# Optimization experiments

Measured on AMD Instinct MI355X. Metric: run time of the kernel, lower is better.

## Reference

```python
import jax, jax.numpy as jnp
import numpy as np
import math

B, N, IN_DIM, HID, HEADS, K, NCLS = 4, 8192, 1024, 512, 8, 16, 2


def setup_inputs() -> dict:
    key = jax.random.key(0)
    ks = jax.random.split(key, 20)
    s = 0.02
    return {
        "inputs": jax.random.normal(ks[0], (B, N, IN_DIM), jnp.float32),
        "W_feat": jax.random.normal(ks[1], (IN_DIM, HID), jnp.float32) * s,
        "b_feat": jnp.zeros((HID,), jnp.float32),
        "w_enc": jax.random.normal(ks[2], (HID, 1), jnp.float32) * s,
        "b_enc": jnp.zeros((1,), jnp.float32),
        "cls_token": jax.random.normal(ks[3], (1, 1, HID), jnp.float32) * s,
        "conv_w": jax.random.normal(ks[4], (HID, 1, 3, 3), jnp.float32) * s,  # depthwise
        "conv_b": jnp.zeros((HID,), jnp.float32),
        "Wq": jax.random.normal(ks[5], (HID, HID), jnp.float32) * s,
        "bq": jnp.zeros((HID,), jnp.float32),
        "Wk": jax.random.normal(ks[6], (HID, HID), jnp.float32) * s,
        "bk": jnp.zeros((HID,), jnp.float32),
        "Wv": jax.random.normal(ks[7], (HID, HID), jnp.float32) * s,
        "bv": jnp.zeros((HID,), jnp.float32),
        "Wo": jax.random.normal(ks[8], (HID, HID), jnp.float32) * s,
        "bo": jnp.zeros((HID,), jnp.float32),
        "Wc": jax.random.normal(ks[9], (HID, NCLS), jnp.float32) * s,
        "bc": jnp.zeros((NCLS,), jnp.float32),
    }


def reference(inputs, W_feat, b_feat, w_enc, b_enc, cls_token, conv_w, conv_b,
              Wq, bq, Wk, bk, Wv, bv, Wo, bo, Wc, bc):
    # ---- feature projection: [B,N,IN] -> [B,N,HID]
    x = inputs @ W_feat + b_feat

    # ---- recalib(option='max'): sigmoid scores, top-k gather, mean -> Q [B,1,HID]
    scores = jax.nn.sigmoid(jnp.squeeze(x @ w_enc + b_enc, -1))  # [B,N]
    _, idx = jax.lax.top_k(scores, K)                             # [B,K]
    topk = jnp.take_along_axis(x, idx[:, :, None], axis=1)        # [B,K,HID]
    Q = jnp.mean(topk, axis=1, keepdims=True)                     # [B,1,HID]

    # ---- shift + act
    x = jax.nn.relu(x - Q)

    # ---- pad to square grid and run depthwise 3x3 conv with residual
    _H = int(math.ceil(math.sqrt(N)))                             # 91
    add = _H * _H - N
    x = jnp.concatenate([x, x[:, :add]], axis=1)                  # [B, _H*_H, HID]
    feat = jnp.transpose(x, (0, 2, 1)).reshape(B, HID, _H, _H)    # [B,C,H,W]
    conv = jax.lax.conv_general_dilated(
        feat, conv_w, window_strides=(1, 1), padding="SAME",
        feature_group_count=HID)
    feat = conv + conv_b[None, :, None, None] + feat
    x = jnp.transpose(feat.reshape(B, HID, _H * _H), (0, 2, 1))   # [B,_H*_H,HID]

    # ---- prepend cls token
    cls = jnp.broadcast_to(cls_token, (B, 1, HID))
    x = jnp.concatenate([cls, x], axis=1)                         # [B,S,HID]

    # ---- MAB(Q, x): multi-head attention with scale 1/sqrt(dim_V)
    d = HID // HEADS
    q = (Q @ Wq + bq).reshape(B, 1, HEADS, d)
    kk = (x @ Wk + bk).reshape(B, -1, HEADS, d)
    v = (x @ Wv + bv).reshape(B, -1, HEADS, d)
    logits_a = jnp.einsum('bqhd,bkhd->bhqk', q, kk) / math.sqrt(HID)
    A = jax.nn.softmax(logits_a, axis=-1)                         # [B,h,1,S]
    O = q + jnp.einsum('bhqk,bkhd->bqhd', A, v)                   # [B,1,h,d]
    O = O.reshape(B, 1, HID)
    O = O + jax.nn.relu(O @ Wo + bo)
    bag = O[:, 0]                                                 # squeeze(1) -> [B,HID]

    return bag @ Wc + bc                                          # logits [B,NCLS]
```

## Files before the change

### kernel.cpp

```cpp
#include <hip/hip_runtime.h>
#include <math.h>

#define BB 4
#define NN 8192
#define IND 1024
#define HID 512
#define HEADS 8
#define KSEL 16
#define NCLS 2
#define HH 91
#define NPIX 8281
#define NTOK 8282
#define MROWS 32768

typedef short short8 __attribute__((ext_vector_type(8)));
typedef float floatx4 __attribute__((ext_vector_type(4)));

__device__ __forceinline__ unsigned short f2bf(float f) {
  union { float f; unsigned u; } v; v.f = f;
  unsigned r = (v.u + 0x7FFFu + ((v.u >> 16) & 1u)) >> 16;
  return (unsigned short)r;
}
__device__ __forceinline__ float bf2f(unsigned short h) {
  union { unsigned u; float f; } v; v.u = ((unsigned)h) << 16;
  return v.f;
}

__device__ __forceinline__ void gld16(const unsigned short* g, void* l) {
  typedef __attribute__((address_space(1))) const void GV;
  typedef __attribute__((address_space(3))) void LV;
  __builtin_amdgcn_global_load_lds((GV*)g, (LV*)l, 16, 0, 0);
}

__global__ void k_u(const float* __restrict__ W, const float* __restrict__ we,
                    float* __restrict__ u) {
  int wave = threadIdx.x >> 6, lane = threadIdx.x & 63;
  int k = blockIdx.x * 4 + wave;
  const float* wr = W + (long)k * HID + lane * 8;
  const float* wer = we + lane * 8;
  float a = 0.f;
#pragma unroll
  for (int i = 0; i < 8; ++i) a = fmaf(wr[i], wer[i], a);
  for (int off = 32; off; off >>= 1) a += __shfl_down(a, off);
  if (lane == 0) u[k] = a;
}

__global__ void k_wt(const float* __restrict__ W, unsigned short* __restrict__ Wt) {
  __shared__ unsigned short s[64][68];
  int kt = blockIdx.x * 64, nt = blockIdx.y * 64;
  int tid = threadIdx.x;
#pragma unroll
  for (int i = 0; i < 16; ++i) {
    int idx = tid + i * 256;
    int kk2 = idx >> 6, nn2 = idx & 63;
    s[nn2][kk2] = f2bf(W[(long)(kt + kk2) * HID + nt + nn2]);
  }
  __syncthreads();
#pragma unroll
  for (int i = 0; i < 16; ++i) {
    int idx = tid + i * 256;
    int nn2 = idx >> 6, kk2 = idx & 63;
    Wt[(long)(nt + nn2) * IND + kt + kk2] = s[nn2][kk2];
  }
}

__global__ void k_cvt(const float* __restrict__ in, const float* __restrict__ u,
                      unsigned short* __restrict__ abf, float* __restrict__ slog) {
  __shared__ float su[IND];
  int tid = threadIdx.x;
  for (int i = tid; i < IND; i += 256) su[i] = u[i];
  __syncthreads();
  int wave = tid >> 6, lane = tid & 63;
  long row = (long)blockIdx.x * 4 + wave;
  const float* ip = in + row * IND;
  unsigned short* op = abf + row * IND;
  float acc = 0.f;
#pragma unroll
  for (int p = 0; p < 4; ++p) {
    int k = p * 256 + lane * 4;
    float4 v = *(const float4*)(ip + k);
    ushort4 o;
    o.x = f2bf(v.x); o.y = f2bf(v.y); o.z = f2bf(v.z); o.w = f2bf(v.w);
    *(ushort4*)(op + k) = o;
    acc += v.x * su[k] + v.y * su[k + 1] + v.z * su[k + 2] + v.w * su[k + 3];
  }
  for (int off = 32; off; off >>= 1) acc += __shfl_down(acc, off);
  if (lane == 0) slog[row] = acc;
}

__global__ __launch_bounds__(512) void k_gemm(const unsigned short* __restrict__ A,
                                              const unsigned short* __restrict__ Bt,
                                              const float* __restrict__ bias,
                                              unsigned short* __restrict__ X) {
  __shared__ unsigned short sA[128 * 32];
  __shared__ unsigned short sB[256 * 32];
  int tid = threadIdx.x;
  int wave = tid >> 6, lane = tid & 63;
  long m0 = (long)blockIdx.x * 128;
  int n0 = blockIdx.y * 256;
  int wm = (wave >> 2) * 64, wn = (wave & 3) * 64;
  int lm = lane & 15, lk = (lane >> 4) * 8;
  floatx4 acc[4][4];
#pragma unroll
  for (int i = 0; i < 4; ++i)
#pragma unroll
    for (int j = 0; j < 4; ++j) acc[i][j] = (floatx4){0.f, 0.f, 0.f, 0.f};

  const unsigned short* gA = A + (m0 + (tid >> 2)) * IND + (tid & 3) * 8;
  const unsigned short* gB = Bt + (long)(n0 + (tid >> 2)) * IND + (tid & 3) * 8;
  char* sAc = (char*)sA + wave * 1024;
  char* sBc = (char*)sB + wave * 1024;

  for (int k0 = 0; k0 < IND; k0 += 32) {
    gld16(gA + k0, sAc);
    gld16(gB + k0, sBc);
    gld16(gB + k0 + 128 * IND, sBc + 8192);
    __syncthreads();
    short8 af[4], bfr[4];
#pragma unroll
    for (int i = 0; i < 4; ++i)
      af[i] = *(const short8*)(sA + (wm + i * 16 + lm) * 32 + lk);
#pragma unroll
    for (int j = 0; j < 4; ++j)
      bfr[j] = *(const short8*)(sB + (wn + j * 16 + lm) * 32 + lk);
#pragma unroll
    for (int i = 0; i < 4; ++i)
#pragma unroll
      for (int j = 0; j < 4; ++j)
        acc[i][j] = __builtin_amdgcn_mfma_f32_16x16x32_bf16(af[i], bfr[j], acc[i][j], 0, 0, 0);
    __syncthreads();
  }
#pragma unroll
  for (int j = 0; j < 4; ++j) {
    int gcol = n0 + wn + j * 16 + lm;
    float bv_ = bias[gcol];
#pragma unroll
    for (int i = 0; i < 4; ++i) {
      long grow = m0 + wm + i * 16 + (lane >> 4) * 4;
#pragma unroll
      for (int r = 0; r < 4; ++r)
        X[(grow + r) * HID + gcol] = f2bf(acc[i][j][r] + bv_);
    }
  }
}

__global__ __launch_bounds__(1024) void k_topq(const float* __restrict__ slog,
                                               const unsigned short* __restrict__ X,
                                               float* __restrict__ Q) {
  __shared__ float sc[NN];
  __shared__ float wvs[16];
  __shared__ int wis[16];
  __shared__ int wi[KSEL];
  int b = blockIdx.x, tid = threadIdx.x;
  int lane = tid & 63, wid = tid >> 6;
  for (int i = tid; i < NN; i += 1024) sc[i] = slog[b * NN + i];
  __syncthreads();
  for (int it = 0; it < KSEL; ++it) {
    float bv = -3.4e38f; int bi = 0x7FFFFFFF;
#pragma unroll
    for (int r = 0; r < 8; ++r) {
      int i = tid + r * 1024;
      float v = sc[i];
      if (v > bv || (v == bv && i < bi)) { bv = v; bi = i; }
    }
    for (int off = 32; off; off >>= 1) {
      float v2 = __shfl_down(bv, off);
      int i2 = __shfl_down(bi, off);
      if (v2 > bv || (v2 == bv && i2 < bi)) { bv = v2; bi = i2; }
    }
    if (lane == 0) { wvs[wid] = bv; wis[wid] = bi; }
    __syncthreads();
    if (tid == 0) {
      float best = wvs[0]; int besti = wis[0];
#pragma unroll
      for (int w = 1; w < 16; ++w)
        if (wvs[w] > best || (wvs[w] == best && wis[w] < besti)) { best = wvs[w]; besti = wis[w]; }
      wi[it] = besti;
      sc[besti] = -3.4e38f;
    }
    __syncthreads();
  }
  if (tid < HID) {
    float s = 0.f;
#pragma unroll
    for (int t2 = 0; t2 < KSEL; ++t2)
      s += bf2f(X[((long)b * NN + wi[t2]) * HID + tid]);
    Q[b * HID + tid] = s * (1.f / KSEL);
  }
}

__global__ void k_conv(const unsigned short* __restrict__ X, const float* __restrict__ Q,
                       const float* __restrict__ cw, const float* __restrict__ cb,
                       unsigned short* __restrict__ XT) {
  int tid = threadIdx.x;
  int b = blockIdx.y;
  int c = tid * 2;
  float w0[9], w1[9];
#pragma unroll
  for (int t = 0; t < 9; ++t) { w0[t] = cw[c * 9 + t]; w1[t] = cw[(c + 1) * 9 + t]; }
  float q0 = Q[b * HID + c], q1 = Q[b * HID + c + 1];
  float cb0 = cb[c], cb1 = cb[c + 1];
  int nbase = blockIdx.x * 8;
  const unsigned short* xb = X + (long)b * NN * HID;
#pragma unroll
  for (int ii = 0; ii < 8; ++ii) {
    int n = nbase + ii;
    if (n >= NPIX) break;
    int h = n / HH, w = n - h * HH;
    float a0 = 0.f, a1 = 0.f, c0v = 0.f, c1v = 0.f;
#pragma unroll
    for (int dy = 0; dy < 3; ++dy) {
      int hh2 = h + dy - 1;
      if (hh2 < 0 || hh2 >= HH) continue;
#pragma unroll
      for (int dx = 0; dx < 3; ++dx) {
        int ww2 = w + dx - 1;
        if (ww2 < 0 || ww2 >= HH) continue;
        int n2 = hh2 * HH + ww2;
        int r = n2 < NN ? n2 : n2 - NN;
        unsigned v = *(const unsigned*)(xb + (long)r * HID + c);
        float f0 = bf2f((unsigned short)(v & 0xFFFF));
        float f1 = bf2f((unsigned short)(v >> 16));
        f0 = fmaxf(f0 - q0, 0.f);
        f1 = fmaxf(f1 - q1, 0.f);
        int t = dy * 3 + dx;
        a0 = fmaf(w0[t], f0, a0);
        a1 = fmaf(w1[t], f1, a1);
        if (t == 4) { c0v = f0; c1v = f1; }
      }
    }
    unsigned out = (unsigned)f2bf(a0 + cb0 + c0v) | ((unsigned)f2bf(a1 + cb1 + c1v) << 16);
    *(unsigned*)(XT + ((long)b * NTOK + 1 + n) * HID + c) = out;
  }
}

__global__ void k_qv(const float* __restrict__ Q, const float* __restrict__ Wq,
                     const float* __restrict__ bq, const float* __restrict__ cls,
                     float* __restrict__ qvec, unsigned short* __restrict__ XT) {
  __shared__ float sq[HID];
  __shared__ float part[4][64];
  int b = blockIdx.y, cblk = blockIdx.x, tid = threadIdx.x;
  for (int i = tid; i < HID; i += 256) sq[i] = Q[b * HID + i];
  __syncthreads();
  int cl = tid & 63, seg = tid >> 6;
  int c = cblk * 64 + cl;
  float a = 0.f;
#pragma unroll 8
  for (int j = seg * 128; j < seg * 128 + 128; ++j)
    a = fmaf(sq[j], Wq[(long)j * HID + c], a);
  part[seg][cl] = a;
  __syncthreads();
  if (seg == 0)
    qvec[b * HID + c] = part[0][cl] + part[1][cl] + part[2][cl] + part[3][cl] + bq[c];
  if (cblk == 0)
    for (int i = tid; i < HID; i += 256)
      XT[(long)b * NTOK * HID + i] = f2bf(cls[i]);
}

__global__ void k_tprep(const float* __restrict__ qvec, const float* __restrict__ Wk,
                        const float* __restrict__ bk, float* __restrict__ tmat,
                        float* __restrict__ bkq) {
  __shared__ float qv[HID];
  int b = blockIdx.y, tid = threadIdx.x;
  for (int i = tid; i < HID; i += 256) qv[i] = qvec[b * HID + i];
  __syncthreads();
  int wave = tid >> 6, lane = tid & 63;
  float q8[8];
#pragma unroll
  for (int i = 0; i < 8; ++i) q8[i] = qv[lane * 8 + i];
#pragma unroll
  for (int jj = 0; jj < 4; ++jj) {
    int j = blockIdx.x * 16 + wave * 4 + jj;
    const float* wr = Wk + (long)j * HID + lane * 8;
    float4 a0 = *(const float4*)wr;
    float4 a1 = *(const float4*)(wr + 4);
    float s = a0.x * q8[0] + a0.y * q8[1] + a0.z * q8[2] + a0.w * q8[3] +
              a1.x * q8[4] + a1.y * q8[5] + a1.z * q8[6] + a1.w * q8[7];
#pragma unroll
    for (int off = 1; off < 8; off <<= 1) s += __shfl_xor(s, off);
    if ((lane & 7) == 0)
      tmat[((long)b * HEADS + (lane >> 3)) * HID + j] = s;
  }
  if (blockIdx.x == 0 && wave == 0) {
    float s = 0.f;
#pragma unroll
    for (int i = 0; i < 8; ++i) s += bk[lane * 8 + i] * q8[i];
#pragma unroll
    for (int off = 1; off < 8; off <<= 1) s += __shfl_xor(s, off);
    if ((lane & 7) == 0) bkq[b * HEADS + (lane >> 3)] = s;
  }
}

__global__ void k_logits(const unsigned short* __restrict__ XT, const float* __restrict__ tmat,
                         const float* __restrict__ bkq, float* __restrict__ logits) {
  __shared__ float st[HEADS * HID];
  __shared__ float sb[HEADS];
  int b = blockIdx.y, tid = threadIdx.x;
  for (int i = tid; i < HEADS * HID; i += 256) st[i] = tmat[(long)b * HEADS * HID + i];
  if (tid < HEADS) sb[tid] = bkq[b * HEADS + tid];
  __syncthreads();
  int wave = tid >> 6, lane = tid & 63;
  float tr[HEADS][8];
#pragma unroll
  for (int h = 0; h < HEADS; ++h)
#pragma unroll
    for (int i = 0; i < 8; ++i) tr[h][i] = st[h * HID + lane * 8 + i];
  float sbr[HEADS];
#pragma unroll
  for (int h = 0; h < HEADS; ++h) sbr[h] = sb[h];

  for (long row = blockIdx.x * 4 + wave; row < NTOK; row += 4L * gridDim.x) {
    const unsigned short* xr = XT + ((long)b * NTOK + row) * HID + lane * 8;
    ushort4 v0 = *(const ushort4*)xr;
    ushort4 v1 = *(const ushort4*)(xr + 4);
    float xf[8] = {bf2f(v0.x), bf2f(v0.y), bf2f(v0.z), bf2f(v0.w),
                   bf2f(v1.x), bf2f(v1.y), bf2f(v1.z), bf2f(v1.w)};
    float acc[HEADS];
#pragma unroll
    for (int h = 0; h < HEADS; ++h) {
      float a = 0.f;
#pragma unroll
      for (int i = 0; i < 8; ++i) a = fmaf(xf[i], tr[h][i], a);
      acc[h] = a;
    }
#pragma unroll
    for (int h = 0; h < HEADS; ++h)
      for (int off = 32; off; off >>= 1) acc[h] += __shfl_down(acc[h], off);
    if (lane == 0) {
#pragma unroll
      for (int h = 0; h < HEADS; ++h)
        logits[((long)b * HEADS + h) * NTOK + row] = (acc[h] + sbr[h]) * 0.044194173824159216f;
    }
  }
}

__global__ void k_soft(float* __restrict__ logits, float* __restrict__ wsum,
                       float* __restrict__ Opart, float* __restrict__ t2) {
  __shared__ float sl[NTOK];
  __shared__ float red[256];
  int bh = blockIdx.x, tid = threadIdx.x;
  int b = bh >> 3, h = bh & 7;
  for (int i = tid; i < HID; i += 256) wsum[(long)bh * HID + i] = 0.f;
  if (tid < 64) {
    Opart[b * HID + h * 64 + tid] = 0.f;
    t2[b * HID + h * 64 + tid] = 0.f;
  }
  float* lp = logits + (long)bh * NTOK;
  for (int i = tid; i < NTOK; i += 256) sl[i] = lp[i];
  __syncthreads();
  float m = -3.4e38f;
  for (int i = tid; i < NTOK; i += 256) m = fmaxf(m, sl[i]);
  red[tid] = m; __syncthreads();
  for (int s = 128; s; s >>= 1) { if (tid < s) red[tid] = fmaxf(red[tid], red[tid + s]); __syncthreads(); }
  m = red[0]; __syncthreads();
  float sm = 0.f;
  for (int i = tid; i < NTOK; i += 256) {
    float e = __expf(sl[i] - m);
    sl[i] = e;
    sm += e;
  }
  red[tid] = sm; __syncthreads();
  for (int s = 128; s; s >>= 1) { if (tid < s) red[tid] += red[tid + s]; __syncthreads(); }
  float inv = 1.f / red[0];
  __syncthreads();
  for (int i = tid; i < NTOK; i += 256) lp[i] = sl[i] * inv;
}

__global__ void k_wsum(const unsigned short* __restrict__ XT, const float* __restrict__ P,
                       float* __restrict__ wsum) {
  __shared__ float pw[HEADS * 64];
  int b = blockIdx.y, tid = threadIdx.x;
  int nbase = blockIdx.x * 64;
  for (int i = tid; i < HEADS * 64; i += 256) {
    int h = i >> 6, nn = i & 63;
    long n = nbase + nn;
    pw[i] = (n < NTOK) ? P[((long)b * HEADS + h) * NTOK + n] : 0.f;
  }
  __syncthreads();
  int c = tid * 2;
  float wa[HEADS][2];
#pragma unroll
  for (int h = 0; h < HEADS; ++h) { wa[h][0] = 0.f; wa[h][1] = 0.f; }
  int lim = NTOK - nbase; if (lim > 64) lim = 64;
  for (int nn = 0; nn < lim; ++nn) {
    unsigned v = *(const unsigned*)(XT + ((long)b * NTOK + nbase + nn) * HID + c);
    float f0 = bf2f((unsigned short)(v & 0xFFFF));
    float f1 = bf2f((unsigned short)(v >> 16));
#pragma unroll
    for (int h = 0; h < HEADS; ++h) {
      float p = pw[h * 64 + nn];
      wa[h][0] = fmaf(p, f0, wa[h][0]);
      wa[h][1] = fmaf(p, f1, wa[h][1]);
    }
  }
#pragma unroll
  for (int h = 0; h < HEADS; ++h) {
    atomicAdd(&wsum[((long)b * HEADS + h) * HID + c], wa[h][0]);
    atomicAdd(&wsum[((long)b * HEADS + h) * HID + c + 1], wa[h][1]);
  }
}

__global__ void k_o1(const float* __restrict__ wsum, const float* __restrict__ Wv,
                     float* __restrict__ Opart) {
  __shared__ float part[2][128];
  int cblk = blockIdx.x, kc = blockIdx.y, b = blockIdx.z;
  int tid = threadIdx.x;
  int cl = tid & 127, seg = tid >> 7;
  int c = cblk * 128 + cl;
  int h = c >> 6;
  const float* wp = wsum + ((long)b * HEADS + h) * HID;
  int j0 = kc * 64 + seg * 32;
  float a = 0.f;
#pragma unroll 8
  for (int j = j0; j < j0 + 32; ++j) a = fmaf(wp[j], Wv[(long)j * HID + c], a);
  part[seg][cl] = a;
  __syncthreads();
  if (seg == 0) atomicAdd(&Opart[b * HID + c], part[0][cl] + part[1][cl]);
}

__global__ void k_o2a(const float* __restrict__ qvec, const float* __restrict__ bv,
                      const float* __restrict__ Opart, const float* __restrict__ Wo,
                      float* __restrict__ t2) {
  __shared__ float part[2][128];
  int cblk = blockIdx.x, kc = blockIdx.y, b = blockIdx.z;
  int tid = threadIdx.x;
  int cl = tid & 127, seg = tid >> 7;
  int c = cblk * 128 + cl;
  int j0 = kc * 64 + seg * 32;
  float a = 0.f;
#pragma unroll 8
  for (int j = j0; j < j0 + 32; ++j) {
    float so = qvec[b * HID + j] + bv[j] + Opart[b * HID + j];
    a = fmaf(so, Wo[(long)j * HID + c], a);
  }
  part[seg][cl] = a;
  __syncthreads();
  if (seg == 0) atomicAdd(&t2[b * HID + c], part[0][cl] + part[1][cl]);
}

__global__ void k_o2b(const float* __restrict__ qvec, const float* __restrict__ bv,
                      const float* __restrict__ Opart, const float* __restrict__ bo,
                      const float* __restrict__ t2, const float* __restrict__ Wc,
                      const float* __restrict__ bc, float* __restrict__ out) {
  __shared__ float r0[256], r1[256];
  int b = blockIdx.x, tid = threadIdx.x;
  float s0 = 0.f, s1 = 0.f;
  for (int c = tid; c < HID; c += 256) {
    float so = qvec[b * HID + c] + bv[c] + Opart[b * HID + c];
    float o2 = so + fmaxf(t2[b * HID + c] + bo[c], 0.f);
    s0 = fmaf(o2, Wc[c * 2], s0);
    s1 = fmaf(o2, Wc[c * 2 + 1], s1);
  }
  r0[tid] = s0; r1[tid] = s1;
  __syncthreads();
  for (int s = 128; s; s >>= 1) {
    if (tid < s) { r0[tid] += r0[tid + s]; r1[tid] += r1[tid + s]; }
    __syncthreads();
  }
  if (tid == 0) {
    out[b * NCLS + 0] = r0[0] + bc[0];
    out[b * NCLS + 1] = r1[0] + bc[1];
  }
}

extern "C" void kernel_launch(void* const* d_in, const int* in_sizes, int n_in,
                              void* d_out, int out_size, void* d_ws, size_t ws_size,
                              hipStream_t stream) {
  const float* inputs = (const float*)d_in[0];
  const float* W_feat = (const float*)d_in[1];
  const float* b_feat = (const float*)d_in[2];
  const float* w_enc  = (const float*)d_in[3];
  const float* cls    = (const float*)d_in[5];
  const float* conv_w = (const float*)d_in[6];
  const float* conv_b = (const float*)d_in[7];
  const float* Wq = (const float*)d_in[8];
  const float* bq = (const float*)d_in[9];
  const float* Wk = (const float*)d_in[10];
  const float* bk = (const float*)d_in[11];
  const float* Wv = (const float*)d_in[12];
  const float* bv = (const float*)d_in[13];
  const float* Wo = (const float*)d_in[14];
  const float* bo = (const float*)d_in[15];
  const float* Wc = (const float*)d_in[16];
  const float* bc = (const float*)d_in[17];
  float* out = (float*)d_out;

  char* ws = (char*)d_ws;
  size_t off = 0;
  auto alloc = [&](size_t bytes) -> void* {
    void* p = ws + off;
    off = (off + bytes + 255) & ~(size_t)255;
    return p;
  };
  unsigned short* abf = (unsigned short*)alloc((size_t)MROWS * IND * 2);
  unsigned short* wt  = (unsigned short*)alloc((size_t)HID * IND * 2);
  unsigned short* X   = (unsigned short*)alloc((size_t)MROWS * HID * 2);
  unsigned short* XT  = (unsigned short*)alloc((size_t)BB * NTOK * HID * 2);
  float* u      = (float*)alloc(IND * 4);
  float* slog   = (float*)alloc((size_t)MROWS * 4);
  float* Q      = (float*)alloc(BB * HID * 4);
  float* qvec   = (float*)alloc(BB * HID * 4);
  float* tmat   = (float*)alloc(BB * HEADS * HID * 4);
  float* bkq    = (float*)alloc(BB * HEADS * 4);
  float* logits = (float*)alloc((size_t)BB * HEADS * NTOK * 4);
  float* wsum   = (float*)alloc(BB * HEADS * HID * 4);
  float* Opart  = (float*)alloc(BB * HID * 4);
  float* t2buf  = (float*)alloc(BB * HID * 4);

  k_u<<<IND / 4, 256, 0, stream>>>(W_feat, w_enc, u);
  k_wt<<<dim3(IND / 64, HID / 64), 256, 0, stream>>>(W_feat, wt);
  k_cvt<<<MROWS / 4, 256, 0, stream>>>(inputs, u, abf, slog);
  k_gemm<<<dim3(MROWS / 128, HID / 256), 512, 0, stream>>>(abf, wt, b_feat, X);
  k_topq<<<BB, 1024, 0, stream>>>(slog, X, Q);
  k_conv<<<dim3((NPIX + 7) / 8, BB), 256, 0, stream>>>(X, Q, conv_w, conv_b, XT);
  k_qv<<<dim3(HID / 64, BB), 256, 0, stream>>>(Q, Wq, bq, cls, qvec, XT);
  k_tprep<<<dim3(HID / 16, BB), 256, 0, stream>>>(qvec, Wk, bk, tmat, bkq);
  k_logits<<<dim3(132, BB), 256, 0, stream>>>(XT, tmat, bkq, logits);
  k_soft<<<BB * HEADS, 256, 0, stream>>>(logits, wsum, Opart, t2buf);
  k_wsum<<<dim3((NTOK + 63) / 64, BB), 256, 0, stream>>>(XT, logits, wsum);
  k_o1<<<dim3(HID / 128, 8, BB), 256, 0, stream>>>(wsum, Wv, Opart);
  k_o2a<<<dim3(HID / 128, 8, BB), 256, 0, stream>>>(qvec, bv, Opart, Wo, t2buf);
  k_o2b<<<BB, 256, 0, stream>>>(qvec, bv, Opart, bo, t2buf, Wc, bc, out);
}
```

Measured before the change: 472.3 us.

## Split top-k into parallel two-stage selection and retile feature GEMM to 128x128

The single-block-per-batch top-16 selection is replaced by a two-stage scheme. Sixteen blocks per batch each pick local top-16 candidates from 512 scores, then one block per batch merges the 256 candidates and gathers the selected rows to form Q. This is meant to remove the serial 16-iteration reduction over 8192 scores that ran on only four blocks. The feature GEMM also moves from 128x256 tiles with 512 threads to 128x128 tiles with 256 threads, processing two 32-wide K slices per barrier. That doubles the grid and halves the number of syncs, at the cost of less B-tile reuse per block.

```diff
diff --git a/kernel.cpp b/kernel.cpp
--- a/kernel.cpp
+++ b/kernel.cpp
@@ -88,17 +88,17 @@
   if (lane == 0) slog[row] = acc;
 }
 
-__global__ __launch_bounds__(512) void k_gemm(const unsigned short* __restrict__ A,
+__global__ __launch_bounds__(256) void k_gemm(const unsigned short* __restrict__ A,
                                               const unsigned short* __restrict__ Bt,
                                               const float* __restrict__ bias,
                                               unsigned short* __restrict__ X) {
-  __shared__ unsigned short sA[128 * 32];
-  __shared__ unsigned short sB[256 * 32];
+  __shared__ unsigned short sA[2][128 * 32];
+  __shared__ unsigned short sB[2][128 * 32];
   int tid = threadIdx.x;
   int wave = tid >> 6, lane = tid & 63;
   long m0 = (long)blockIdx.x * 128;
-  int n0 = blockIdx.y * 256;
-  int wm = (wave >> 2) * 64, wn = (wave & 3) * 64;
+  int n0 = blockIdx.y * 128;
+  int wm = (wave >> 1) * 64, wn = (wave & 1) * 64;
   int lm = lane & 15, lk = (lane >> 4) * 8;
   floatx4 acc[4][4];
 #pragma unroll
@@ -108,26 +108,36 @@
 
   const unsigned short* gA = A + (m0 + (tid >> 2)) * IND + (tid & 3) * 8;
   const unsigned short* gB = Bt + (long)(n0 + (tid >> 2)) * IND + (tid & 3) * 8;
-  char* sAc = (char*)sA + wave * 1024;
-  char* sBc = (char*)sB + wave * 1024;
-
-  for (int k0 = 0; k0 < IND; k0 += 32) {
-    gld16(gA + k0, sAc);
-    gld16(gB + k0, sBc);
-    gld16(gB + k0 + 128 * IND, sBc + 8192);
-    __syncthreads();
-    short8 af[4], bfr[4];
-#pragma unroll
-    for (int i = 0; i < 4; ++i)
-      af[i] = *(const short8*)(sA + (wm + i * 16 + lm) * 32 + lk);
-#pragma unroll
-    for (int j = 0; j < 4; ++j)
-      bfr[j] = *(const short8*)(sB + (wn + j * 16 + lm) * 32 + lk);
-#pragma unroll
-    for (int i = 0; i < 4; ++i)
+  char* a0 = (char*)sA[0] + wave * 1024;
+  char* a1 = (char*)sA[1] + wave * 1024;
+  char* b0 = (char*)sB[0] + wave * 1024;
+  char* b1 = (char*)sB[1] + wave * 1024;
+
+  for (int k0 = 0; k0 < IND; k0 += 64) {
+    gld16(gA + k0, a0);
+    gld16(gA + k0 + 64 * IND, a0 + 4096);
+    gld16(gA + k0 + 32, a1);
+    gld16(gA + k0 + 32 + 64 * IND, a1 + 4096);
+    gld16(gB + k0, b0);
+    gld16(gB + k0 + 64 * IND, b0 + 4096);
+    gld16(gB + k0 + 32, b1);
+    gld16(gB + k0 + 32 + 64 * IND, b1 + 4096);
+    __syncthreads();
+#pragma unroll
+    for (int ks = 0; ks < 2; ++ks) {
+      short8 af[4], bfr[4];
+#pragma unroll
+      for (int i = 0; i < 4; ++i)
+        af[i] = *(const short8*)(sA[ks] + (wm + i * 16 + lm) * 32 + lk);
 #pragma unroll
       for (int j = 0; j < 4; ++j)
-        acc[i][j] = __builtin_amdgcn_mfma_f32_16x16x32_bf16(af[i], bfr[j], acc[i][j], 0, 0, 0);
+        bfr[j] = *(const short8*)(sB[ks] + (wn + j * 16 + lm) * 32 + lk);
+#pragma unroll
+      for (int i = 0; i < 4; ++i)
+#pragma unroll
+        for (int j = 0; j < 4; ++j)
+          acc[i][j] = __builtin_amdgcn_mfma_f32_16x16x32_bf16(af[i], bfr[j], acc[i][j], 0, 0, 0);
+    }
     __syncthreads();
   }
 #pragma unroll
@@ -144,48 +154,82 @@
   }
 }
 
-__global__ __launch_bounds__(1024) void k_topq(const float* __restrict__ slog,
-                                               const unsigned short* __restrict__ X,
-                                               float* __restrict__ Q) {
-  __shared__ float sc[NN];
-  __shared__ float wvs[16];
-  __shared__ int wis[16];
-  __shared__ int wi[KSEL];
-  int b = blockIdx.x, tid = threadIdx.x;
+__global__ void k_topa(const float* __restrict__ slog, float* __restrict__ cval,
+                       int* __restrict__ cidx) {
+  __shared__ float sc[512];
+  __shared__ float wv[4];
+  __shared__ int wiL[4];
+  int b = blockIdx.y, blk = blockIdx.x, tid = threadIdx.x;
+  int base = b * NN + blk * 512;
+  sc[tid] = slog[base + tid];
+  sc[tid + 256] = slog[base + tid + 256];
+  __syncthreads();
   int lane = tid & 63, wid = tid >> 6;
-  for (int i = tid; i < NN; i += 1024) sc[i] = slog[b * NN + i];
-  __syncthreads();
   for (int it = 0; it < KSEL; ++it) {
-    float bv = -3.4e38f; int bi = 0x7FFFFFFF;
-#pragma unroll
-    for (int r = 0; r < 8; ++r) {
-      int i = tid + r * 1024;
-      float v = sc[i];
-      if (v > bv || (v == bv && i < bi)) { bv = v; bi = i; }
-    }
+    float v0 = sc[tid], v1 = sc[tid + 256];
+    float bv; int bi;
+    if (v1 > v0) { bv = v1; bi = tid + 256; } else { bv = v0; bi = tid; }
     for (int off = 32; off; off >>= 1) {
       float v2 = __shfl_down(bv, off);
       int i2 = __shfl_down(bi, off);
       if (v2 > bv || (v2 == bv && i2 < bi)) { bv = v2; bi = i2; }
     }
-    if (lane == 0) { wvs[wid] = bv; wis[wid] = bi; }
+    if (lane == 0) { wv[wid] = bv; wiL[wid] = bi; }
     __syncthreads();
     if (tid == 0) {
-      float best = wvs[0]; int besti = wis[0];
-#pragma unroll
-      for (int w = 1; w < 16; ++w)
-        if (wvs[w] > best || (wvs[w] == best && wis[w] < besti)) { best = wvs[w]; besti = wis[w]; }
+      float best = wv[0]; int besti = wiL[0];
+#pragma unroll
+      for (int w = 1; w < 4; ++w)
+        if (wv[w] > best || (wv[w] == best && wiL[w] < besti)) { best = wv[w]; besti = wiL[w]; }
+      cval[(b * 16 + blk) * 16 + it] = best;
+      cidx[(b * 16 + blk) * 16 + it] = blk * 512 + besti;
+      sc[besti] = -3.4e38f;
+    }
+    __syncthreads();
+  }
+}
+
+__global__ void k_topb(const float* __restrict__ cval, const int* __restrict__ cidx,
+                       const unsigned short* __restrict__ X, float* __restrict__ Q) {
+  __shared__ float cv[256];
+  __shared__ int ci[256];
+  __shared__ float wv[4];
+  __shared__ int wiL[4];
+  __shared__ int wsl[4];
+  __shared__ int wi[KSEL];
+  int b = blockIdx.x, tid = threadIdx.x;
+  cv[tid] = cval[b * 256 + tid];
+  ci[tid] = cidx[b * 256 + tid];
+  __syncthreads();
+  int lane = tid & 63, wid = tid >> 6;
+  for (int it = 0; it < KSEL; ++it) {
+    float bv = cv[tid]; int bi = ci[tid]; int sl = tid;
+    for (int off = 32; off; off >>= 1) {
+      float v2 = __shfl_down(bv, off);
+      int i2 = __shfl_down(bi, off);
+      int s2 = __shfl_down(sl, off);
+      if (v2 > bv || (v2 == bv && i2 < bi)) { bv = v2; bi = i2; sl = s2; }
+    }
+    if (lane == 0) { wv[wid] = bv; wiL[wid] = bi; wsl[wid] = sl; }
+    __syncthreads();
+    if (tid == 0) {
+      float best = wv[0]; int besti = wiL[0]; int bests = wsl[0];
+#pragma unroll
+      for (int w = 1; w < 4; ++w)
+        if (wv[w] > best || (wv[w] == best && wiL[w] < besti)) {
+          best = wv[w]; besti = wiL[w]; bests = wsl[w];
+        }
       wi[it] = besti;
-      sc[besti] = -3.4e38f;
-    }
-    __syncthreads();
-  }
-  if (tid < HID) {
+      cv[bests] = -3.4e38f;
+    }
+    __syncthreads();
+  }
+  for (int c = tid; c < HID; c += 256) {
     float s = 0.f;
 #pragma unroll
     for (int t2 = 0; t2 < KSEL; ++t2)
-      s += bf2f(X[((long)b * NN + wi[t2]) * HID + tid]);
-    Q[b * HID + tid] = s * (1.f / KSEL);
+      s += bf2f(X[((long)b * NN + wi[t2]) * HID + c]);
+    Q[b * HID + c] = s * (1.f / KSEL);
   }
 }
 
@@ -498,6 +542,8 @@
   unsigned short* XT  = (unsigned short*)alloc((size_t)BB * NTOK * HID * 2);
   float* u      = (float*)alloc(IND * 4);
   float* slog   = (float*)alloc((size_t)MROWS * 4);
+  float* cvalb  = (float*)alloc(BB * 256 * 4);
+  int*   cidxb  = (int*)alloc(BB * 256 * 4);
   float* Q      = (float*)alloc(BB * HID * 4);
   float* qvec   = (float*)alloc(BB * HID * 4);
   float* tmat   = (float*)alloc(BB * HEADS * HID * 4);
@@ -510,8 +556,9 @@
   k_u<<<IND / 4, 256, 0, stream>>>(W_feat, w_enc, u);
   k_wt<<<dim3(IND / 64, HID / 64), 256, 0, stream>>>(W_feat, wt);
   k_cvt<<<MROWS / 4, 256, 0, stream>>>(inputs, u, abf, slog);
-  k_gemm<<<dim3(MROWS / 128, HID / 256), 512, 0, stream>>>(abf, wt, b_feat, X);
-  k_topq<<<BB, 1024, 0, stream>>>(slog, X, Q);
+  k_gemm<<<dim3(MROWS / 128, HID / 128), 256, 0, stream>>>(abf, wt, b_feat, X);
+  k_topa<<<dim3(16, BB), 256, 0, stream>>>(slog, cvalb, cidxb);
+  k_topb<<<BB, 256, 0, stream>>>(cvalb, cidxb, X, Q);
   k_conv<<<dim3((NPIX + 7) / 8, BB), 256, 0, stream>>>(X, Q, conv_w, conv_b, XT);
   k_qv<<<dim3(HID / 64, BB), 256, 0, stream>>>(Q, Wq, bq, cls, qvec, XT);
   k_tprep<<<dim3(HID / 16, BB), 256, 0, stream>>>(qvec, Wk, bk, tmat, bkq);
```

Result: no change. 465.9 us (-1.4%).
